# Optimization experiments

Measured on AMD Instinct MI355X. Metric: run time of the kernel, lower is better.

## Reference

```python
import jax, jax.numpy as jnp
import numpy as np


def setup_inputs() -> dict:
    key = jax.random.key(0)
    ks = jax.random.split(key, 11)
    B, T, I, H, O = 64, 256, 1024, 1024, 1024
    s_g = 1.0 / np.sqrt(I + H)  # torch Linear init scale (uniform); use scaled normal
    s_v = 1.0 / np.sqrt(H)
    return {
        "inputs": jax.random.normal(ks[0], (B, T, I), jnp.float32),
        "Wf_w": jax.random.normal(ks[1], (H, I + H), jnp.float32) * s_g,
        "Wf_b": jax.random.normal(ks[2], (H,), jnp.float32) * s_g,
        "Wi_w": jax.random.normal(ks[3], (H, I + H), jnp.float32) * s_g,
        "Wi_b": jax.random.normal(ks[4], (H,), jnp.float32) * s_g,
        "Wc_w": jax.random.normal(ks[5], (H, I + H), jnp.float32) * s_g,
        "Wc_b": jax.random.normal(ks[6], (H,), jnp.float32) * s_g,
        "Wo_w": jax.random.normal(ks[7], (H, I + H), jnp.float32) * s_g,
        "Wo_b": jax.random.normal(ks[8], (H,), jnp.float32) * s_g,
        "V_w": jax.random.normal(ks[9], (O, H), jnp.float32) * s_v,
        "V_b": jax.random.normal(ks[10], (O,), jnp.float32) * s_v,
    }


def reference(inputs, Wf_w, Wf_b, Wi_w, Wi_b, Wc_w, Wc_b, Wo_w, Wo_b, V_w, V_b):
    B, T, I = inputs.shape
    H = Wf_w.shape[0]
    # Fuse the four gate linears into one GEMM (mathematically identical).
    W_all = jnp.concatenate([Wf_w, Wi_w, Wo_w, Wc_w], axis=0)  # (4H, I+H)
    b_all = jnp.concatenate([Wf_b, Wi_b, Wo_b, Wc_b], axis=0)  # (4H,)

    def step(carry, x_t):  # x_t: (B, I)
        c, h = carry
        combined = jnp.concatenate([x_t, h], axis=1)            # (B, I+H)
        gates = combined @ W_all.T + b_all                      # (B, 4H)
        f, i, o, g = jnp.split(gates, 4, axis=1)
        f = jax.nn.sigmoid(f)
        i = jax.nn.sigmoid(i)
        o = jax.nn.sigmoid(o)
        g = jnp.tanh(g)
        c = f * c + i * g
        h = o * jnp.tanh(c)
        return (c, h), None

    c0 = jnp.zeros((B, H), inputs.dtype)
    h0 = jnp.zeros((B, H), inputs.dtype)
    (c, h), _ = jax.lax.scan(step, (c0, h0), jnp.swapaxes(inputs, 0, 1))
    last_out = h @ V_w.T + V_b  # outputs[:, -1, :] only depends on final h
    return (c, h, last_out)
```

## Files before the change

kernel.cpp:

```cpp
#include <hip/hip_runtime.h>
#include <hip/hip_bf16.h>

typedef __bf16 bf16x8 __attribute__((ext_vector_type(8)));
typedef float f32x4 __attribute__((ext_vector_type(4)));
typedef unsigned long long u64;

#define TSTEPS 256
#define NB 64
#define ID 1024
#define HD 1024
#define KD 2048

#define WOFF 0ull
#define VOFF 16777216ull
#define BOFF 18874368ull
#define HMOFF 18890752ull
#define XBOFF 52580352ull

#define SENT 0xFFFFFFFFu

__device__ __forceinline__ unsigned short f2b(float f) {
    unsigned int u = __float_as_uint(f);
    unsigned int r = (u + 0x7fffu + ((u >> 16) & 1u)) >> 16;
    return (unsigned short)r;
}

__device__ __forceinline__ bf16x8 as_frag(uint4 u) {
    union { uint4 u; bf16x8 v; } c; c.u = u; return c.v;
}

__device__ __forceinline__ uint4 ld_b128_cp(const void* p) {
    uint4 r;
    asm volatile("global_load_dwordx4 %0, %1, off sc0 sc1" : "=v"(r) : "v"(p));
    return r;
}
__device__ __forceinline__ uint4 ld_b128(const void* p) {
    uint4 r;
    asm volatile("global_load_dwordx4 %0, %1, off" : "=v"(r) : "v"(p));
    return r;
}

__global__ void cvt_x(const float* __restrict__ in, unsigned short* __restrict__ out) {
    size_t i = ((size_t)blockIdx.x * 256 + threadIdx.x) * 8;
    int t = (int)(i >> 16);
    int b = (int)(i >> 10) & 63;
    int k = (int)i & 1023;
    const float* src = in + ((size_t)b << 18) + ((size_t)t << 10) + k;
    float4 a = *(const float4*)src;
    float4 bb = *(const float4*)(src + 4);
    union { unsigned short h[8]; uint4 u; } o;
    o.h[0] = f2b(a.x); o.h[1] = f2b(a.y); o.h[2] = f2b(a.z); o.h[3] = f2b(a.w);
    o.h[4] = f2b(bb.x); o.h[5] = f2b(bb.y); o.h[6] = f2b(bb.z); o.h[7] = f2b(bb.w);
    *(uint4*)(out + i) = o.u;
}

__global__ void cvt_w(const float* __restrict__ Wf, const float* __restrict__ Wi,
                      const float* __restrict__ Wo, const float* __restrict__ Wc,
                      const float* __restrict__ bf_, const float* __restrict__ bi_,
                      const float* __restrict__ bo_, const float* __restrict__ bc_,
                      unsigned short* __restrict__ Wr, float* __restrict__ bias_r) {
    int idx = blockIdx.x * 256 + threadIdx.x;
    int np = idx >> 8;
    int k  = (idx & 255) * 8;
    int g = np & 3, h = np >> 2;
    const float* W = (g == 0) ? Wf : (g == 1) ? Wi : (g == 2) ? Wo : Wc;
    const float* src = W + (size_t)h * KD + k;
    float4 a = *(const float4*)src;
    float4 b = *(const float4*)(src + 4);
    union { unsigned short h[8]; uint4 u; } o;
    o.h[0] = f2b(a.x); o.h[1] = f2b(a.y); o.h[2] = f2b(a.z); o.h[3] = f2b(a.w);
    o.h[4] = f2b(b.x); o.h[5] = f2b(b.y); o.h[6] = f2b(b.z); o.h[7] = f2b(b.w);
    *(uint4*)(Wr + (size_t)np * KD + k) = o.u;
    if (k == 0) {
        const float* B = (g == 0) ? bf_ : (g == 1) ? bi_ : (g == 2) ? bo_ : bc_;
        bias_r[np] = B[h];
    }
}

__global__ void cvt_v(const float* __restrict__ V, unsigned short* __restrict__ out) {
    size_t i = ((size_t)blockIdx.x * blockDim.x + threadIdx.x) * 8;
    float4 a = *(const float4*)(V + i);
    float4 b = *(const float4*)(V + i + 4);
    union { unsigned short h[8]; uint4 u; } o;
    o.h[0] = f2b(a.x); o.h[1] = f2b(a.y); o.h[2] = f2b(a.z); o.h[3] = f2b(a.w);
    o.h[4] = f2b(b.x); o.h[5] = f2b(b.y); o.h[6] = f2b(b.z); o.h[7] = f2b(b.w);
    *(uint4*)(out + i) = o.u;
}

__global__ void init_h(unsigned short* __restrict__ h0) {
    size_t i = ((size_t)blockIdx.x * blockDim.x + threadIdx.x) * 8;
    uint4 z = {0, 0, 0, 0};
    *(uint4*)(h0 + i) = z;
}

__global__ void init_sent(unsigned short* __restrict__ h1) {
    size_t i = ((size_t)blockIdx.x * blockDim.x + threadIdx.x) * 8;
    uint4 s = {SENT, SENT, SENT, SENT};
    *(uint4*)(h1 + i) = s;
}

__device__ __forceinline__ float sigf(float x) {
    return 1.0f / (1.0f + __expf(-x));
}
__device__ __forceinline__ float tanhfast(float x) {
    return 2.0f / (1.0f + __expf(-2.0f * x)) - 1.0f;
}

__launch_bounds__(512, 1)
__global__ void lstm_core(const unsigned short* __restrict__ xb,
                          const unsigned short* __restrict__ Wr,
                          const float* __restrict__ bias_r,
                          unsigned short* __restrict__ hm,
                          const unsigned short* __restrict__ Vw,
                          const float* __restrict__ Vbias,
                          float* __restrict__ out) {
    __shared__ float gxp[2][8][64][20];

    const int bid  = blockIdx.x;
    const int tid  = threadIdx.x;
    const int wave = tid >> 6;
    const int lane = tid & 63;
    const int lrow = lane & 15;
    const int kq   = (lane >> 4) << 3;
    const int n0   = bid << 4;
    const int qr   = (lane >> 4) << 2;

    const int ct   = tid - 256;
    const int ob   = (ct >> 2) & 63;
    const int lhc  = ct & 3;
    const int hcol = (bid << 2) + lhc;
    float4 bb = {0, 0, 0, 0};
    if (tid >= 256) bb = *(const float4*)&bias_r[n0 + (lhc << 2)];

    const bool isx = wave < 4;
    const unsigned short* wptr = Wr + (size_t)(n0 + lrow) * KD + (wave << 8) + kq;

    uint4 wfrag[8];
    #pragma unroll
    for (int kk8 = 0; kk8 < 8; ++kk8)
        wfrag[kk8] = ld_b128(wptr + kk8 * 32);
    asm volatile("s_waitcnt vmcnt(0)" ::: "memory");
    __builtin_amdgcn_sched_barrier(0);

    int koff = 0;
    if (!isx) koff = ((wave - 4) << 8) + kq;
    const int xko = (wave << 8) + kq;

    float c_reg = 0.f;
    float hlast = 0.f;

    for (int t = 0; t < TSTEPS; ++t) {
        const int par = t & 1;
        f32x4 acc[4];
        #pragma unroll
        for (int m = 0; m < 4; ++m) acc[m] = (f32x4){0, 0, 0, 0};

        if (isx) {
            const unsigned short* xt = xb + ((size_t)t << 16);
            #pragma unroll
            for (int kk8 = 0; kk8 < 8; ++kk8)
                #pragma unroll
                for (int m = 0; m < 4; ++m)
                    acc[m] = __builtin_amdgcn_mfma_f32_16x16x32_bf16(
                        *(const bf16x8*)(xt + (size_t)(m * 16 + lrow) * 1024 + xko + kk8 * 32),
                        as_frag(wfrag[kk8]), acc[m], 0, 0, 0);
        } else {
            const unsigned short* hmt = hm + ((size_t)t << 16);
            const int c8b = koff >> 3;
            uint4 hv[8][4];
            int it = 0;
            for (;;) {
                #pragma unroll
                for (int j = 0; j < 8; ++j)
                    #pragma unroll
                    for (int m = 0; m < 4; ++m)
                        hv[j][m] = ld_b128_cp(hmt + (size_t)(c8b + j * 4) * 512 + (m * 16 + lrow) * 8);
                asm volatile("s_waitcnt vmcnt(0)" ::: "memory");
                __builtin_amdgcn_sched_barrier(0);
                unsigned int bad = 0;
                #pragma unroll
                for (int j = 0; j < 8; ++j)
                    #pragma unroll
                    for (int m = 0; m < 4; ++m)
                        bad |= (hv[j][m].x == SENT) | (hv[j][m].y == SENT) |
                               (hv[j][m].z == SENT) | (hv[j][m].w == SENT);
                if (__all(bad == 0) || ++it > (1 << 15)) break;
            }
            __builtin_amdgcn_sched_barrier(0);
            #pragma unroll
            for (int j = 0; j < 8; ++j)
                #pragma unroll
                for (int m = 0; m < 4; ++m)
                    acc[m] = __builtin_amdgcn_mfma_f32_16x16x32_bf16(as_frag(hv[j][m]),
                                                                     as_frag(wfrag[j]), acc[m], 0, 0, 0);
        }

        #pragma unroll
        for (int m = 0; m < 4; ++m)
            #pragma unroll
            for (int r = 0; r < 4; ++r)
                gxp[par][wave][m * 16 + qr + r][lrow] = acc[m][r];
        __syncthreads();

        if (tid >= 256) {
            float fpre = bb.x, ipre = bb.y, opre = bb.z, gpre = bb.w;
            #pragma unroll
            for (int w = 0; w < 8; ++w) {
                float4 s = *(const float4*)&gxp[par][w][ob][lhc << 2];
                fpre += s.x; ipre += s.y; opre += s.z; gpre += s.w;
            }
            float fg = sigf(fpre);
            float ig = sigf(ipre);
            float og = sigf(opre);
            float gg = tanhfast(gpre);
            c_reg = fg * c_reg + ig * gg;
            float hh = og * tanhfast(c_reg);
            if (t == TSTEPS - 1) hlast = hh;

            unsigned int hb = f2b(hh);
            unsigned int p1 = __shfl_down(hb, 1);
            unsigned int p2 = __shfl_down(hb, 2);
            unsigned int p3 = __shfl_down(hb, 3);
            if ((lane & 3) == 0) {
                u64 v = (u64)hb | ((u64)p1 << 16) | ((u64)p2 << 32) | ((u64)p3 << 48);
                unsigned short* dst = hm + ((size_t)(t + 1) << 16)
                                       + (size_t)(bid >> 1) * 512 + (size_t)ob * 8 + ((bid & 1) << 2);
                asm volatile("global_store_dwordx2 %0, %1, off sc0 sc1" :: "v"(dst), "v"(v) : "memory");
            }
        }
    }

    if (tid >= 256) {
        out[(size_t)ob * HD + hcol] = c_reg;
        out[65536 + (size_t)ob * HD + hcol] = hlast;
    }

    if (bid < 64) {
        f32x4 acc[4];
        #pragma unroll
        for (int m = 0; m < 4; ++m) acc[m] = (f32x4){0, 0, 0, 0};
        const int ko2 = (wave << 7) + kq;
        const unsigned short* vp = Vw + (size_t)(n0 + lrow) * HD + ko2;
        const unsigned short* hmt = hm + ((size_t)TSTEPS << 16);
        const int c8b = ko2 >> 3;
        uint4 pw[4], pv[4][4];
        #pragma unroll
        for (int j = 0; j < 4; ++j)
            pw[j] = ld_b128(vp + j * 32);
        int it = 0;
        for (;;) {
            #pragma unroll
            for (int j = 0; j < 4; ++j)
                #pragma unroll
                for (int m = 0; m < 4; ++m)
                    pv[j][m] = ld_b128_cp(hmt + (size_t)(c8b + j * 4) * 512 + (m * 16 + lrow) * 8);
            asm volatile("s_waitcnt vmcnt(0)" ::: "memory");
            __builtin_amdgcn_sched_barrier(0);
            unsigned int bad = 0;
            #pragma unroll
            for (int j = 0; j < 4; ++j)
                #pragma unroll
                for (int m = 0; m < 4; ++m)
                    bad |= (pv[j][m].x == SENT) | (pv[j][m].y == SENT) |
                           (pv[j][m].z == SENT) | (pv[j][m].w == SENT);
            if (__all(bad == 0) || ++it > (1 << 14)) break;
        }
        __builtin_amdgcn_sched_barrier(0);
        #pragma unroll
        for (int j = 0; j < 4; ++j)
            #pragma unroll
            for (int m = 0; m < 4; ++m)
                acc[m] = __builtin_amdgcn_mfma_f32_16x16x32_bf16(as_frag(pv[j][m]),
                                                                 as_frag(pw[j]), acc[m], 0, 0, 0);
        #pragma unroll
        for (int m = 0; m < 4; ++m)
            #pragma unroll
            for (int r = 0; r < 4; ++r)
                gxp[0][wave][m * 16 + qr + r][lrow] = acc[m][r];
        __syncthreads();
        if (tid >= 256) {
            float4 vb = *(const float4*)&Vbias[n0 + (lhc << 2)];
            float4 res = vb;
            #pragma unroll
            for (int w = 0; w < 8; ++w) {
                float4 s = *(const float4*)&gxp[0][w][ob][lhc << 2];
                res.x += s.x; res.y += s.y; res.z += s.z; res.w += s.w;
            }
            *(float4*)&out[131072 + (size_t)ob * 1024 + n0 + (lhc << 2)] = res;
        }
    }
}

extern "C" void kernel_launch(void* const* d_in, const int* in_sizes, int n_in,
                              void* d_out, int out_size, void* d_ws, size_t ws_size,
                              hipStream_t stream) {
    const float* x   = (const float*)d_in[0];
    const float* Wf  = (const float*)d_in[1];
    const float* bf_ = (const float*)d_in[2];
    const float* Wi  = (const float*)d_in[3];
    const float* bi_ = (const float*)d_in[4];
    const float* Wc  = (const float*)d_in[5];
    const float* bc_ = (const float*)d_in[6];
    const float* Wo  = (const float*)d_in[7];
    const float* bo_ = (const float*)d_in[8];
    const float* Vw  = (const float*)d_in[9];
    const float* Vb  = (const float*)d_in[10];

    char* ws = (char*)d_ws;
    unsigned short* Wr     = (unsigned short*)(ws + WOFF);
    unsigned short* Vbf    = (unsigned short*)(ws + VOFF);
    float*          bias_r = (float*)(ws + BOFF);
    unsigned short* hm     = (unsigned short*)(ws + HMOFF);
    unsigned short* xbb    = (unsigned short*)(ws + XBOFF);
    float*          outp   = (float*)d_out;

    cvt_x <<<8192, 256, 0, stream>>>(x, xbb);
    cvt_w <<<4096, 256, 0, stream>>>(Wf, Wi, Wo, Wc, bf_, bi_, bo_, bc_, Wr, bias_r);
    cvt_v <<<512, 256, 0, stream>>>(Vw, Vbf);
    init_h<<<32, 256, 0, stream>>>(hm);
    init_sent<<<8192, 256, 0, stream>>>(hm + 65536);

    void* args[] = {&xbb, &Wr, &bias_r, &hm, &Vbf, (void*)&Vb, &outp};
    hipLaunchCooperativeKernel((const void*)lstm_core, dim3(256), dim3(512), args, 0, stream);
}
```

Baseline: 1.719 ms.

## Replace sentinel polling of h data with per-block step flags and split h loads

Each block now publishes a per-block step counter after writing its slice of h, and consumer waves poll only the flags of the blocks they depend on instead of repeatedly reloading the full h tile with cache-bypassing loads and checking for sentinel values. Once the flags are ready, h is read with normal loads in two halves so the second half's loads overlap the first half's MFMAs. This also drops the 8192-block sentinel init kernel and the double-buffered LDS gate buffer. In exchange it adds an extra __syncthreads plus a store wait and a flag store on every step.

```diff
diff --git a/kernel.cpp b/kernel.cpp
--- a/kernel.cpp
+++ b/kernel.cpp
@@ -15,9 +15,8 @@
 #define VOFF 16777216ull
 #define BOFF 18874368ull
 #define HMOFF 18890752ull
+#define BAROFF 52576256ull
 #define XBOFF 52580352ull
-
-#define SENT 0xFFFFFFFFu
 
 __device__ __forceinline__ unsigned short f2b(float f) {
     unsigned int u = __float_as_uint(f);
@@ -29,14 +28,21 @@
     union { uint4 u; bf16x8 v; } c; c.u = u; return c.v;
 }
 
-__device__ __forceinline__ uint4 ld_b128_cp(const void* p) {
-    uint4 r;
-    asm volatile("global_load_dwordx4 %0, %1, off sc0 sc1" : "=v"(r) : "v"(p));
-    return r;
-}
 __device__ __forceinline__ uint4 ld_b128(const void* p) {
     uint4 r;
     asm volatile("global_load_dwordx4 %0, %1, off" : "=v"(r) : "v"(p));
+    return r;
+}
+__device__ __forceinline__ unsigned int ld_dw_cp(const unsigned int* p) {
+    unsigned int r;
+    asm volatile("global_load_dword %0, %1, off sc0 sc1\n\ts_waitcnt vmcnt(0)"
+                 : "=v"(r) : "v"(p) : "memory");
+    return r;
+}
+__device__ __forceinline__ uint4 ld_dw4_cp(const unsigned int* p) {
+    uint4 r;
+    asm volatile("global_load_dwordx4 %0, %1, off sc0 sc1\n\ts_waitcnt vmcnt(0)"
+                 : "=v"(r) : "v"(p) : "memory");
     return r;
 }
 
@@ -93,10 +99,8 @@
     *(uint4*)(h0 + i) = z;
 }
 
-__global__ void init_sent(unsigned short* __restrict__ h1) {
-    size_t i = ((size_t)blockIdx.x * blockDim.x + threadIdx.x) * 8;
-    uint4 s = {SENT, SENT, SENT, SENT};
-    *(uint4*)(h1 + i) = s;
+__global__ void init_bar(unsigned int* __restrict__ flags) {
+    flags[threadIdx.x] = 0;
 }
 
 __device__ __forceinline__ float sigf(float x) {
@@ -113,8 +117,9 @@
                           unsigned short* __restrict__ hm,
                           const unsigned short* __restrict__ Vw,
                           const float* __restrict__ Vbias,
-                          float* __restrict__ out) {
-    __shared__ float gxp[2][8][64][20];
+                          float* __restrict__ out,
+                          unsigned int* __restrict__ flags) {
+    __shared__ float gxp[8][64][20];
 
     const int bid  = blockIdx.x;
     const int tid  = threadIdx.x;
@@ -142,15 +147,15 @@
     asm volatile("s_waitcnt vmcnt(0)" ::: "memory");
     __builtin_amdgcn_sched_barrier(0);
 
+    const int w4 = wave - 4;
     int koff = 0;
-    if (!isx) koff = ((wave - 4) << 8) + kq;
+    if (!isx) koff = (w4 << 8) + kq;
     const int xko = (wave << 8) + kq;
 
     float c_reg = 0.f;
     float hlast = 0.f;
 
     for (int t = 0; t < TSTEPS; ++t) {
-        const int par = t & 1;
         f32x4 acc[4];
         #pragma unroll
         for (int m = 0; m < 4; ++m) acc[m] = (f32x4){0, 0, 0, 0};
@@ -165,48 +170,70 @@
                         *(const bf16x8*)(xt + (size_t)(m * 16 + lrow) * 1024 + xko + kk8 * 32),
                         as_frag(wfrag[kk8]), acc[m], 0, 0, 0);
         } else {
+            const unsigned int* fp = flags + (w4 << 6) + lane;
+            int it = 0;
+            while (ld_dw_cp(fp) < (unsigned int)t || !__all(1)) {
+                if (++it > (1 << 20)) break;
+                __builtin_amdgcn_s_sleep(1);
+            }
+            {
+                int it2 = 0;
+                for (;;) {
+                    unsigned int f = ld_dw_cp(fp);
+                    if (__all(f >= (unsigned int)t) || ++it2 > (1 << 20)) break;
+                    __builtin_amdgcn_s_sleep(1);
+                }
+            }
+            __builtin_amdgcn_sched_barrier(0);
+
             const unsigned short* hmt = hm + ((size_t)t << 16);
             const int c8b = koff >> 3;
-            uint4 hv[8][4];
-            int it = 0;
-            for (;;) {
-                #pragma unroll
-                for (int j = 0; j < 8; ++j)
-                    #pragma unroll
-                    for (int m = 0; m < 4; ++m)
-                        hv[j][m] = ld_b128_cp(hmt + (size_t)(c8b + j * 4) * 512 + (m * 16 + lrow) * 8);
-                asm volatile("s_waitcnt vmcnt(0)" ::: "memory");
-                __builtin_amdgcn_sched_barrier(0);
-                unsigned int bad = 0;
-                #pragma unroll
-                for (int j = 0; j < 8; ++j)
-                    #pragma unroll
-                    for (int m = 0; m < 4; ++m)
-                        bad |= (hv[j][m].x == SENT) | (hv[j][m].y == SENT) |
-                               (hv[j][m].z == SENT) | (hv[j][m].w == SENT);
-                if (__all(bad == 0) || ++it > (1 << 15)) break;
-            }
+            uint4 hA[4][4], hB[4][4];
+            #pragma unroll
+            for (int j = 0; j < 4; ++j)
+                #pragma unroll
+                for (int m = 0; m < 4; ++m)
+                    hA[j][m] = ld_b128(hmt + (size_t)(c8b + j * 4) * 512 + (m * 16 + lrow) * 8);
+            asm volatile("s_waitcnt vmcnt(0)" ::: "memory");
             __builtin_amdgcn_sched_barrier(0);
-            #pragma unroll
-            for (int j = 0; j < 8; ++j)
-                #pragma unroll
-                for (int m = 0; m < 4; ++m)
-                    acc[m] = __builtin_amdgcn_mfma_f32_16x16x32_bf16(as_frag(hv[j][m]),
+
+            #pragma unroll
+            for (int j = 0; j < 4; ++j)
+                #pragma unroll
+                for (int m = 0; m < 4; ++m)
+                    hB[j][m] = ld_b128(hmt + (size_t)(c8b + (j + 4) * 4) * 512 + (m * 16 + lrow) * 8);
+            __builtin_amdgcn_sched_barrier(0);
+
+            #pragma unroll
+            for (int j = 0; j < 4; ++j)
+                #pragma unroll
+                for (int m = 0; m < 4; ++m)
+                    acc[m] = __builtin_amdgcn_mfma_f32_16x16x32_bf16(as_frag(hA[j][m]),
                                                                      as_frag(wfrag[j]), acc[m], 0, 0, 0);
+
+            asm volatile("s_waitcnt vmcnt(0)" ::: "memory");
+            __builtin_amdgcn_sched_barrier(0);
+
+            #pragma unroll
+            for (int j = 0; j < 4; ++j)
+                #pragma unroll
+                for (int m = 0; m < 4; ++m)
+                    acc[m] = __builtin_amdgcn_mfma_f32_16x16x32_bf16(as_frag(hB[j][m]),
+                                                                     as_frag(wfrag[j + 4]), acc[m], 0, 0, 0);
         }
 
         #pragma unroll
         for (int m = 0; m < 4; ++m)
             #pragma unroll
             for (int r = 0; r < 4; ++r)
-                gxp[par][wave][m * 16 + qr + r][lrow] = acc[m][r];
+                gxp[wave][m * 16 + qr + r][lrow] = acc[m][r];
         __syncthreads();
 
         if (tid >= 256) {
             float fpre = bb.x, ipre = bb.y, opre = bb.z, gpre = bb.w;
             #pragma unroll
             for (int w = 0; w < 8; ++w) {
-                float4 s = *(const float4*)&gxp[par][w][ob][lhc << 2];
+                float4 s = *(const float4*)&gxp[w][ob][lhc << 2];
                 fpre += s.x; ipre += s.y; opre += s.z; gpre += s.w;
             }
             float fg = sigf(fpre);
@@ -227,6 +254,14 @@
                                        + (size_t)(bid >> 1) * 512 + (size_t)ob * 8 + ((bid & 1) << 2);
                 asm volatile("global_store_dwordx2 %0, %1, off sc0 sc1" :: "v"(dst), "v"(v) : "memory");
             }
+            asm volatile("s_waitcnt vmcnt(0)" ::: "memory");
+        }
+        __syncthreads();
+
+        if (tid == 256) {
+            unsigned int* fdst = flags + bid;
+            unsigned int fv = (unsigned int)(t + 1);
+            asm volatile("global_store_dword %0, %1, off sc0 sc1" :: "v"(fdst), "v"(fv) : "memory");
         }
     }
 
@@ -236,6 +271,17 @@
     }
 
     if (bid < 64) {
+        {
+            const unsigned int* fp = flags + (lane << 2);
+            int it = 0;
+            for (;;) {
+                uint4 f = ld_dw4_cp(fp);
+                bool ok = f.x >= 256u && f.y >= 256u && f.z >= 256u && f.w >= 256u;
+                if (__all(ok) || ++it > (1 << 20)) break;
+                __builtin_amdgcn_s_sleep(1);
+            }
+        }
+        __builtin_amdgcn_sched_barrier(0);
         f32x4 acc[4];
         #pragma unroll
         for (int m = 0; m < 4; ++m) acc[m] = (f32x4){0, 0, 0, 0};
@@ -245,26 +291,13 @@
         const int c8b = ko2 >> 3;
         uint4 pw[4], pv[4][4];
         #pragma unroll
-        for (int j = 0; j < 4; ++j)
+        for (int j = 0; j < 4; ++j) {
             pw[j] = ld_b128(vp + j * 32);
-        int it = 0;
-        for (;;) {
-            #pragma unroll
-            for (int j = 0; j < 4; ++j)
-                #pragma unroll
-                for (int m = 0; m < 4; ++m)
-                    pv[j][m] = ld_b128_cp(hmt + (size_t)(c8b + j * 4) * 512 + (m * 16 + lrow) * 8);
-            asm volatile("s_waitcnt vmcnt(0)" ::: "memory");
-            __builtin_amdgcn_sched_barrier(0);
-            unsigned int bad = 0;
-            #pragma unroll
-            for (int j = 0; j < 4; ++j)
-                #pragma unroll
-                for (int m = 0; m < 4; ++m)
-                    bad |= (pv[j][m].x == SENT) | (pv[j][m].y == SENT) |
-                           (pv[j][m].z == SENT) | (pv[j][m].w == SENT);
-            if (__all(bad == 0) || ++it > (1 << 14)) break;
-        }
+            #pragma unroll
+            for (int m = 0; m < 4; ++m)
+                pv[j][m] = ld_b128(hmt + (size_t)(c8b + j * 4) * 512 + (m * 16 + lrow) * 8);
+        }
+        asm volatile("s_waitcnt vmcnt(0)" ::: "memory");
         __builtin_amdgcn_sched_barrier(0);
         #pragma unroll
         for (int j = 0; j < 4; ++j)
@@ -276,14 +309,14 @@
         for (int m = 0; m < 4; ++m)
             #pragma unroll
             for (int r = 0; r < 4; ++r)
-                gxp[0][wave][m * 16 + qr + r][lrow] = acc[m][r];
+                gxp[wave][m * 16 + qr + r][lrow] = acc[m][r];
         __syncthreads();
         if (tid >= 256) {
             float4 vb = *(const float4*)&Vbias[n0 + (lhc << 2)];
             float4 res = vb;
             #pragma unroll
             for (int w = 0; w < 8; ++w) {
-                float4 s = *(const float4*)&gxp[0][w][ob][lhc << 2];
+                float4 s = *(const float4*)&gxp[w][ob][lhc << 2];
                 res.x += s.x; res.y += s.y; res.z += s.z; res.w += s.w;
             }
             *(float4*)&out[131072 + (size_t)ob * 1024 + n0 + (lhc << 2)] = res;
@@ -311,6 +344,7 @@
     unsigned short* Vbf    = (unsigned short*)(ws + VOFF);
     float*          bias_r = (float*)(ws + BOFF);
     unsigned short* hm     = (unsigned short*)(ws + HMOFF);
+    unsigned int*   flags  = (unsigned int*)(ws + BAROFF);
     unsigned short* xbb    = (unsigned short*)(ws + XBOFF);
     float*          outp   = (float*)d_out;
 
@@ -318,8 +352,8 @@
     cvt_w <<<4096, 256, 0, stream>>>(Wf, Wi, Wo, Wc, bf_, bi_, bo_, bc_, Wr, bias_r);
     cvt_v <<<512, 256, 0, stream>>>(Vw, Vbf);
     init_h<<<32, 256, 0, stream>>>(hm);
-    init_sent<<<8192, 256, 0, stream>>>(hm + 65536);
-
-    void* args[] = {&xbb, &Wr, &bias_r, &hm, &Vbf, (void*)&Vb, &outp};
+    init_bar<<<1, 256, 0, stream>>>(flags);
+
+    void* args[] = {&xbb, &Wr, &bias_r, &hm, &Vbf, (void*)&Vb, &outp, &flags};
     hipLaunchCooperativeKernel((const void*)lstm_core, dim3(256), dim3(512), args, 0, stream);
 }
```

Measured after the change: 2.134 ms. 24.2% more time.
